# Performance work log

Hardware: AMD Instinct MI355X
Metric: run time of the kernel (lower is better)

## Reference

```python
import jax, jax.numpy as jnp
import numpy as np

DIM = 384
NUM_HEADS = 6
HEAD_DIM = DIM // NUM_HEADS
SCALE = HEAD_DIM ** -0.5


def setup_inputs() -> dict:
    key = jax.random.key(0)
    k_x, k_wqkv, k_bqkv, k_wp, k_bp = jax.random.split(key, 5)
    B, N, D = 16, 1024, DIM
    s = 0.02
    return {
        "x": jax.random.normal(k_x, (B, N, D), dtype=jnp.float32),
        "w_qkv": jax.random.normal(k_wqkv, (D, 3 * D), dtype=jnp.float32) * s,
        "b_qkv": jax.random.normal(k_bqkv, (3 * D,), dtype=jnp.float32) * s,
        "w_proj": jax.random.normal(k_wp, (D, D), dtype=jnp.float32) * s,
        "b_proj": jax.random.normal(k_bp, (D,), dtype=jnp.float32) * s,
    }


def reference(x, w_qkv, b_qkv, w_proj, b_proj):
    b, n, d = x.shape
    qkv = x @ w_qkv + b_qkv                               # (B, N, 3D)
    qkv = qkv.reshape(b, n, 3, NUM_HEADS, HEAD_DIM)
    qkv = jnp.transpose(qkv, (2, 0, 3, 1, 4))             # (3, B, H, N, hd)
    q, k, v = qkv[0], qkv[1], qkv[2]
    attn = jnp.einsum("bhqd,bhkd->bhqk", q, k) * SCALE    # (B, H, N, N)
    attn = jax.nn.softmax(attn, axis=-1)
    out = jnp.einsum("bhqk,bhkd->bhqd", attn, v)          # (B, H, N, hd)
    out = jnp.transpose(out, (0, 2, 1, 3)).reshape(b, n, d)
    return out @ w_proj + b_proj
```

## Files before the change

### kernel.cpp

```cpp
#include <hip/hip_runtime.h>

typedef __attribute__((ext_vector_type(8))) short short8;
typedef __attribute__((ext_vector_type(4))) float float4_t;
typedef __attribute__((ext_vector_type(4))) unsigned int uint4_t;

#define MFMA16(A, B, C) __builtin_amdgcn_mfma_f32_16x16x32_bf16(A, B, C, 0, 0, 0)

__device__ __forceinline__ unsigned short f2bf(float f) {
  unsigned int u = __builtin_bit_cast(unsigned int, f);
  u += 0x7FFFu + ((u >> 16) & 1u);
  return (unsigned short)(u >> 16);
}

__device__ __forceinline__ void gload16(const unsigned short* g, unsigned short* l) {
  __builtin_amdgcn_global_load_lds(
      (const __attribute__((address_space(1))) unsigned int*)(g),
      (__attribute__((address_space(3))) unsigned int*)(l), 16, 0, 0);
}

__global__ __launch_bounds__(256) void prep(
    const float* __restrict__ x, const float* __restrict__ w_qkv,
    const float* __restrict__ w_proj, unsigned short* __restrict__ xb,
    unsigned short* __restrict__ wqkvT, unsigned short* __restrict__ wprojT) {
  __shared__ unsigned short tile[32][33];
  const int bid = blockIdx.x, tid = threadIdx.x;
  if (bid < 6144) {
    const int i = bid * 256 + tid;
    float4 v = reinterpret_cast<const float4*>(x)[i];
    ushort4 r;
    r.x = f2bf(v.x); r.y = f2bf(v.y); r.z = f2bf(v.z); r.w = f2bf(v.w);
    reinterpret_cast<ushort4*>(xb)[i] = r;
    return;
  }
  const float* w; unsigned short* wT; int E, t;
  if (bid < 6576) { t = bid - 6144; w = w_qkv; wT = wqkvT; E = 1152; }
  else            { t = bid - 6576; w = w_proj; wT = wprojT; E = 384; }
  const int tiles_e = E >> 5;
  const int td = t / tiles_e, te = t - td * tiles_e;
  const int r = tid >> 3, c4 = (tid & 7) * 4;
  float4 v = *reinterpret_cast<const float4*>(&w[(size_t)(td * 32 + r) * E + te * 32 + c4]);
  tile[r][c4 + 0] = f2bf(v.x);
  tile[r][c4 + 1] = f2bf(v.y);
  tile[r][c4 + 2] = f2bf(v.z);
  tile[r][c4 + 3] = f2bf(v.w);
  __syncthreads();
  ushort4 o;
  o.x = tile[c4 + 0][r]; o.y = tile[c4 + 1][r];
  o.z = tile[c4 + 2][r]; o.w = tile[c4 + 3][r];
  *reinterpret_cast<ushort4*>(&wT[(size_t)(te * 32 + r) * 384 + td * 32 + c4]) = o;
}

__global__ __launch_bounds__(256, 2) void gemm_qkv(
    const unsigned short* __restrict__ xb,
    const unsigned short* __restrict__ wT,
    const float* __restrict__ bias,
    unsigned short* __restrict__ qb,
    unsigned short* __restrict__ kb,
    unsigned short* __restrict__ vt) {
  __shared__ alignas(16) char smem[65536];
  const int tid = threadIdx.x;
  const int wg = (blockIdx.x & 7) * 144 + (blockIdx.x >> 3);
  const int bm = wg / 9, bn = wg - bm * 9;
  const int m0 = bm * 128, n0 = bn * 128;
  const int lane = tid & 63, wid = tid >> 6;
  const int lr = lane & 15, lg = lane >> 4;
  const int wm = wid >> 1, wn = wid & 1;
  float4_t acc[4][4] = {};

  const unsigned short* asrc[4];
  const unsigned short* bsrc[4];
  int dstoff[4];
#pragma unroll
  for (int i = 0; i < 4; ++i) {
    const int idx = tid + i * 256;
    const int r = idx >> 3, c8 = idx & 7;
    const int cc = (c8 ^ (r & 7)) * 8;
    asrc[i] = xb + (size_t)(m0 + r) * 384 + cc;
    bsrc[i] = wT + (size_t)(n0 + r) * 384 + cc;
    dstoff[i] = idx * 16;
  }
  const int rxor = (lr & 7) << 4;

#pragma unroll
  for (int i = 0; i < 4; ++i) {
    gload16(asrc[i], (unsigned short*)(smem + dstoff[i]));
    gload16(bsrc[i], (unsigned short*)(smem + 32768 + dstoff[i]));
  }
  __syncthreads();

#pragma unroll
  for (int kt = 0; kt < 6; ++kt) {
    const int cur = kt & 1;
    if (kt < 5) {
      const int nb = (cur ^ 1) * 16384;
#pragma unroll
      for (int i = 0; i < 4; ++i) {
        gload16(asrc[i] + (kt + 1) * 64, (unsigned short*)(smem + nb + dstoff[i]));
        gload16(bsrc[i] + (kt + 1) * 64, (unsigned short*)(smem + 32768 + nb + dstoff[i]));
      }
    }
    const char* Ab = smem + cur * 16384;
    const char* Bb = smem + 32768 + cur * 16384;
#pragma unroll
    for (int kk = 0; kk < 2; ++kk) {
      short8 a[4], b[4];
#pragma unroll
      for (int f = 0; f < 4; ++f) {
        a[f] = *reinterpret_cast<const short8*>(
            Ab + (wm * 64 + f * 16 + lr) * 128 + ((kk * 64 + lg * 16) ^ rxor));
        b[f] = *reinterpret_cast<const short8*>(
            Bb + (wn * 64 + f * 16 + lr) * 128 + ((kk * 64 + lg * 16) ^ rxor));
      }
#pragma unroll
      for (int mf = 0; mf < 4; ++mf)
#pragma unroll
        for (int nf = 0; nf < 4; ++nf)
          acc[mf][nf] = MFMA16(a[mf], b[nf], acc[mf][nf]);
    }
    __syncthreads();
  }

#pragma unroll
  for (int nf = 0; nf < 4; ++nf) {
    const int e = n0 + wn * 64 + nf * 16 + lr;
    const float bv = bias[e];
    const int which = e / 384;
    const int d = e - which * 384;
    const int h = d >> 6, hi = d & 63;
#pragma unroll
    for (int mf = 0; mf < 4; ++mf) {
      const int mm0 = m0 + wm * 64 + mf * 16 + lg * 4;
      const int b0 = mm0 >> 10, n_b = mm0 & 1023;
      const size_t bh = (size_t)(b0 * 6 + h);
      if (which == 2) {
        const int np = (n_b & ~31) | ((n_b & 12) << 1) | ((n_b & 16) >> 2);
        ushort4 sv;
        sv.x = f2bf(acc[mf][nf][0] + bv);
        sv.y = f2bf(acc[mf][nf][1] + bv);
        sv.z = f2bf(acc[mf][nf][2] + bv);
        sv.w = f2bf(acc[mf][nf][3] + bv);
        *reinterpret_cast<ushort4*>(&vt[bh * 65536 + (size_t)hi * 1024 + np]) = sv;
      } else {
        unsigned short* dst = (which == 0) ? qb : kb;
#pragma unroll
        for (int j = 0; j < 4; ++j) {
          float val = acc[mf][nf][j] + bv;
          if (which == 0) val *= 0.125f;
          dst[bh * 65536 + (size_t)(n_b + j) * 64 + hi] = f2bf(val);
        }
      }
    }
  }
}

__global__ __launch_bounds__(256, 6) void attn(
    const unsigned short* __restrict__ qb,
    const unsigned short* __restrict__ kb,
    const unsigned short* __restrict__ vt,
    unsigned short* __restrict__ ab) {
  __shared__ alignas(16) char smem[16384];
  const int tid = threadIdx.x;
  const int wg = (blockIdx.x & 7) * 192 + (blockIdx.x >> 3);
  const int bh = wg >> 4, qt = wg & 15;
  const int lane = tid & 63, wid = tid >> 6;
  const int lr = lane & 15, lg = lane >> 4;
  const size_t base = (size_t)bh * 65536;
  const unsigned short* qp = qb + base;
  const unsigned short* kp = kb + base;
  const unsigned short* vp = vt + base;
  const int q0 = qt * 64 + wid * 16;

  short8 aq0 = *reinterpret_cast<const short8*>(&qp[(size_t)(q0 + lr) * 64 + lg * 8]);
  short8 aq1 = *reinterpret_cast<const short8*>(&qp[(size_t)(q0 + lr) * 64 + 32 + lg * 8]);

  const int rK = tid >> 3;
  const int cK = (((tid & 7) * 16) ^ ((rK & 7) << 4)) >> 1;
  const int rV = tid >> 2;
  const int cV = (((tid & 3) * 16) ^ ((rV & 3) << 4)) >> 1;
  const unsigned short* ksrc = kp + rK * 64 + cK;
  const unsigned short* vsrc = vp + rV * 1024 + cV;
  unsigned short* kdst0 = (unsigned short*)(smem + wid * 1024);
  unsigned short* vdst0 = (unsigned short*)(smem + 8192 + wid * 1024);

  const int kxor = (lr & 7) << 4;
  const int vxor = (lr & 3) << 4;

  float lsum = 0.f;
  float4_t o[4] = {};

  gload16(ksrc, kdst0);
  gload16(vsrc, vdst0);
  __syncthreads();

  for (int kt = 0; kt < 32; ++kt) {
    const int cur = kt & 1;
    if (kt < 31) {
      const int nb = (cur ^ 1) * 4096;
      gload16(ksrc + (kt + 1) * 2048, (unsigned short*)((char*)kdst0 + nb));
      gload16(vsrc + (kt + 1) * 32, (unsigned short*)((char*)vdst0 + nb));
    }
    const char* kbase = smem + cur * 4096;
    const char* vbase = smem + 8192 + cur * 4096;

    short8 bk[2][2], bv[4];
#pragma unroll
    for (int kf = 0; kf < 2; ++kf)
#pragma unroll
      for (int h = 0; h < 2; ++h)
        bk[kf][h] = *reinterpret_cast<const short8*>(
            kbase + (kf * 16 + lr) * 128 + ((h * 64 + lg * 16) ^ kxor));
#pragma unroll
    for (int f = 0; f < 4; ++f)
      bv[f] = *reinterpret_cast<const short8*>(
          vbase + (f * 16 + lr) * 64 + ((lg * 16) ^ vxor));

    float4_t s[2] = {};
#pragma unroll
    for (int kf = 0; kf < 2; ++kf) {
      s[kf] = MFMA16(bk[kf][0], aq0, s[kf]);
      s[kf] = MFMA16(bk[kf][1], aq1, s[kf]);
    }
    unsigned int dw[4];
#pragma unroll
    for (int kf = 0; kf < 2; ++kf) {
      const float p0 = __expf(s[kf][0]);
      const float p1 = __expf(s[kf][1]);
      const float p2 = __expf(s[kf][2]);
      const float p3 = __expf(s[kf][3]);
      lsum += (p0 + p1) + (p2 + p3);
      dw[kf * 2]     = (unsigned int)f2bf(p0) | ((unsigned int)f2bf(p1) << 16);
      dw[kf * 2 + 1] = (unsigned int)f2bf(p2) | ((unsigned int)f2bf(p3) << 16);
    }
    uint4_t pw;
    pw[0] = dw[0]; pw[1] = dw[1]; pw[2] = dw[2]; pw[3] = dw[3];
    const short8 pa = __builtin_bit_cast(short8, pw);
#pragma unroll
    for (int f = 0; f < 4; ++f)
      o[f] = MFMA16(pa, bv[f], o[f]);

    __syncthreads();
  }

  float t = lsum;
  t += __shfl_xor(t, 16);
  t += __shfl_xor(t, 32);
  const float inv = 1.f / t;

  const int b = bh / 6, h = bh - b * 6;
  float invj[4];
#pragma unroll
  for (int j = 0; j < 4; ++j)
    invj[j] = __shfl(inv, lg * 4 + j);
#pragma unroll
  for (int f = 0; f < 4; ++f)
#pragma unroll
    for (int j = 0; j < 4; ++j) {
      const int q = q0 + lg * 4 + j;
      ab[(size_t)(b * 1024 + q) * 384 + h * 64 + f * 16 + lr] =
          f2bf(o[f][j] * invj[j]);
    }
}

__global__ __launch_bounds__(256, 3) void gemm_proj(
    const unsigned short* __restrict__ ab,
    const unsigned short* __restrict__ wT,
    const float* __restrict__ bias,
    float* __restrict__ out) {
  __shared__ alignas(16) char smem[49152];
  const int tid = threadIdx.x;
  const int wg = (blockIdx.x & 7) * 96 + (blockIdx.x >> 3);
  const int bm = wg / 3, bn = wg - bm * 3;
  const int m0 = bm * 64, n0 = bn * 128;
  const int lane = tid & 63, wid = tid >> 6;
  const int lr = lane & 15, lg = lane >> 4;
  const int wm = wid >> 1, wn = wid & 1;
  float4_t acc[2][4] = {};

  const unsigned short* asrc[2];
  const unsigned short* bsrc[4];
  int adst[2], bdst[4];
#pragma unroll
  for (int i = 0; i < 2; ++i) {
    const int idx = tid + i * 256;
    const int r = idx >> 3, c8 = idx & 7;
    asrc[i] = ab + (size_t)(m0 + r) * 384 + (c8 ^ (r & 7)) * 8;
    adst[i] = idx * 16;
  }
#pragma unroll
  for (int i = 0; i < 4; ++i) {
    const int idx = tid + i * 256;
    const int r = idx >> 3, c8 = idx & 7;
    bsrc[i] = wT + (size_t)(n0 + r) * 384 + (c8 ^ (r & 7)) * 8;
    bdst[i] = idx * 16;
  }
  const int rxor = (lr & 7) << 4;

#pragma unroll
  for (int i = 0; i < 2; ++i) gload16(asrc[i], (unsigned short*)(smem + adst[i]));
#pragma unroll
  for (int i = 0; i < 4; ++i) gload16(bsrc[i], (unsigned short*)(smem + 16384 + bdst[i]));
  __syncthreads();

#pragma unroll
  for (int kt = 0; kt < 6; ++kt) {
    const int cur = kt & 1;
    if (kt < 5) {
#pragma unroll
      for (int i = 0; i < 2; ++i)
        gload16(asrc[i] + (kt + 1) * 64, (unsigned short*)(smem + (cur ^ 1) * 8192 + adst[i]));
#pragma unroll
      for (int i = 0; i < 4; ++i)
        gload16(bsrc[i] + (kt + 1) * 64, (unsigned short*)(smem + 16384 + (cur ^ 1) * 16384 + bdst[i]));
    }
    const char* Ab = smem + cur * 8192;
    const char* Bb = smem + 16384 + cur * 16384;
#pragma unroll
    for (int kk = 0; kk < 2; ++kk) {
      short8 a[2], b[4];
#pragma unroll
      for (int f = 0; f < 2; ++f)
        a[f] = *reinterpret_cast<const short8*>(
            Ab + (wm * 32 + f * 16 + lr) * 128 + ((kk * 64 + lg * 16) ^ rxor));
#pragma unroll
      for (int f = 0; f < 4; ++f)
        b[f] = *reinterpret_cast<const short8*>(
            Bb + (wn * 64 + f * 16 + lr) * 128 + ((kk * 64 + lg * 16) ^ rxor));
#pragma unroll
      for (int mf = 0; mf < 2; ++mf)
#pragma unroll
        for (int nf = 0; nf < 4; ++nf)
          acc[mf][nf] = MFMA16(a[mf], b[nf], acc[mf][nf]);
    }
    __syncthreads();
  }

#pragma unroll
  for (int nf = 0; nf < 4; ++nf) {
    const int e = n0 + wn * 64 + nf * 16 + lr;
    const float bv = bias[e];
#pragma unroll
    for (int mf = 0; mf < 2; ++mf) {
#pragma unroll
      for (int j = 0; j < 4; ++j) {
        const int mm = m0 + wm * 32 + mf * 16 + lg * 4 + j;
        out[(size_t)mm * 384 + e] = acc[mf][nf][j] + bv;
      }
    }
  }
}

extern "C" void kernel_launch(void* const* d_in, const int* in_sizes, int n_in,
                              void* d_out, int out_size, void* d_ws, size_t ws_size,
                              hipStream_t stream) {
  const float* x      = (const float*)d_in[0];
  const float* w_qkv  = (const float*)d_in[1];
  const float* b_qkv  = (const float*)d_in[2];
  const float* w_proj = (const float*)d_in[3];
  const float* b_proj = (const float*)d_in[4];
  float* out = (float*)d_out;

  char* ws = (char*)d_ws;
  unsigned short* xb     = (unsigned short*)(ws);
  unsigned short* wqkvT  = (unsigned short*)(ws + 12582912);
  unsigned short* wprojT = (unsigned short*)(ws + 13467648);
  unsigned short* qb     = (unsigned short*)(ws + 13762560);
  unsigned short* kb     = (unsigned short*)(ws + 26345472);
  unsigned short* vt     = (unsigned short*)(ws + 38928384);
  unsigned short* ab     = xb;

  prep<<<6720, 256, 0, stream>>>(x, w_qkv, w_proj, xb, wqkvT, wprojT);
  gemm_qkv<<<1152, 256, 0, stream>>>(xb, wqkvT, b_qkv, qb, kb, vt);
  attn<<<1536, 256, 0, stream>>>(qb, kb, vt, ab);
  gemm_proj<<<768, 256, 0, stream>>>(ab, wprojT, b_proj, out);
}
```

Measured before the change: 96.11 us.

## Vectorize QKV/proj epilogues, enlarge attention tiles, use exp2 and packed bf16 conversion

In the QKV and projection GEMMs, the MFMA operands are swapped for Q/K and the output tiles so each lane holds four consecutive columns, letting the epilogues issue 8-byte bf16 and 16-byte float stores with a vector bias load. The attention kernel moves to 512-thread blocks covering 128 queries and 64-key tiles, which halves the number of K/V loads and barriers per query. Q is prescaled by log2(e)/8 so the softmax can use the hardware exp2 directly. Probabilities are packed with v_cvt_pk_bf16_f32, and the row sum is taken from the rounded bf16 values. The larger blocks double LDS use and change occupancy, and the unnormalized exp with no max subtraction is kept.

```diff
diff --git a/kernel.cpp b/kernel.cpp
--- a/kernel.cpp
+++ b/kernel.cpp
@@ -5,6 +5,8 @@
 typedef __attribute__((ext_vector_type(4))) unsigned int uint4_t;
 
 #define MFMA16(A, B, C) __builtin_amdgcn_mfma_f32_16x16x32_bf16(A, B, C, 0, 0, 0)
+
+#define QSCALE 0.1803368801111168f
 
 __device__ __forceinline__ unsigned short f2bf(float f) {
   unsigned int u = __builtin_bit_cast(unsigned int, f);
@@ -111,133 +113,166 @@
         b[f] = *reinterpret_cast<const short8*>(
             Bb + (wn * 64 + f * 16 + lr) * 128 + ((kk * 64 + lg * 16) ^ rxor));
       }
-#pragma unroll
-      for (int mf = 0; mf < 4; ++mf)
-#pragma unroll
-        for (int nf = 0; nf < 4; ++nf)
-          acc[mf][nf] = MFMA16(a[mf], b[nf], acc[mf][nf]);
+      if (bn < 6) {
+#pragma unroll
+        for (int mf = 0; mf < 4; ++mf)
+#pragma unroll
+          for (int nf = 0; nf < 4; ++nf)
+            acc[mf][nf] = MFMA16(b[nf], a[mf], acc[mf][nf]);
+      } else {
+#pragma unroll
+        for (int mf = 0; mf < 4; ++mf)
+#pragma unroll
+          for (int nf = 0; nf < 4; ++nf)
+            acc[mf][nf] = MFMA16(a[mf], b[nf], acc[mf][nf]);
+      }
     }
     __syncthreads();
   }
 
-#pragma unroll
-  for (int nf = 0; nf < 4; ++nf) {
-    const int e = n0 + wn * 64 + nf * 16 + lr;
-    const float bv = bias[e];
-    const int which = e / 384;
-    const int d = e - which * 384;
-    const int h = d >> 6, hi = d & 63;
-#pragma unroll
-    for (int mf = 0; mf < 4; ++mf) {
-      const int mm0 = m0 + wm * 64 + mf * 16 + lg * 4;
-      const int b0 = mm0 >> 10, n_b = mm0 & 1023;
-      const size_t bh = (size_t)(b0 * 6 + h);
-      if (which == 2) {
+  if (bn < 6) {
+    const int whichk = (bn >= 3);
+    unsigned short* dst = whichk ? kb : qb;
+    const float sc = whichk ? 1.f : QSCALE;
+#pragma unroll
+    for (int nf = 0; nf < 4; ++nf) {
+      const int e0 = n0 + wn * 64 + nf * 16 + lg * 4;
+      const int d0 = e0 - whichk * 384;
+      const int h = d0 >> 6, hi0 = d0 & 63;
+      const float4 bv4 = *reinterpret_cast<const float4*>(&bias[e0]);
+#pragma unroll
+      for (int mf = 0; mf < 4; ++mf) {
+        const int mm = m0 + wm * 64 + mf * 16 + lr;
+        const int b0 = mm >> 10, n_b = mm & 1023;
+        const size_t bhh = (size_t)(b0 * 6 + h);
+        ushort4 sv;
+        sv.x = f2bf((acc[mf][nf][0] + bv4.x) * sc);
+        sv.y = f2bf((acc[mf][nf][1] + bv4.y) * sc);
+        sv.z = f2bf((acc[mf][nf][2] + bv4.z) * sc);
+        sv.w = f2bf((acc[mf][nf][3] + bv4.w) * sc);
+        *reinterpret_cast<ushort4*>(&dst[bhh * 65536 + (size_t)n_b * 64 + hi0]) = sv;
+      }
+    }
+  } else {
+#pragma unroll
+    for (int nf = 0; nf < 4; ++nf) {
+      const int e = n0 + wn * 64 + nf * 16 + lr;
+      const float bv = bias[e];
+      const int d = e - 768;
+      const int h = d >> 6, hi = d & 63;
+#pragma unroll
+      for (int mf = 0; mf < 4; ++mf) {
+        const int mm0 = m0 + wm * 64 + mf * 16 + lg * 4;
+        const int b0 = mm0 >> 10, n_b = mm0 & 1023;
+        const size_t bhh = (size_t)(b0 * 6 + h);
         const int np = (n_b & ~31) | ((n_b & 12) << 1) | ((n_b & 16) >> 2);
         ushort4 sv;
         sv.x = f2bf(acc[mf][nf][0] + bv);
         sv.y = f2bf(acc[mf][nf][1] + bv);
         sv.z = f2bf(acc[mf][nf][2] + bv);
         sv.w = f2bf(acc[mf][nf][3] + bv);
-        *reinterpret_cast<ushort4*>(&vt[bh * 65536 + (size_t)hi * 1024 + np]) = sv;
-      } else {
-        unsigned short* dst = (which == 0) ? qb : kb;
-#pragma unroll
-        for (int j = 0; j < 4; ++j) {
-          float val = acc[mf][nf][j] + bv;
-          if (which == 0) val *= 0.125f;
-          dst[bh * 65536 + (size_t)(n_b + j) * 64 + hi] = f2bf(val);
-        }
-      }
-    }
-  }
-}
-
-__global__ __launch_bounds__(256, 6) void attn(
+        *reinterpret_cast<ushort4*>(&vt[bhh * 65536 + (size_t)hi * 1024 + np]) = sv;
+      }
+    }
+  }
+}
+
+__global__ __launch_bounds__(512, 6) void attn(
     const unsigned short* __restrict__ qb,
     const unsigned short* __restrict__ kb,
     const unsigned short* __restrict__ vt,
     unsigned short* __restrict__ ab) {
-  __shared__ alignas(16) char smem[16384];
+  __shared__ alignas(16) char smem[32768];
   const int tid = threadIdx.x;
-  const int wg = (blockIdx.x & 7) * 192 + (blockIdx.x >> 3);
-  const int bh = wg >> 4, qt = wg & 15;
+  const int wg = (blockIdx.x & 7) * 96 + (blockIdx.x >> 3);
+  const int bh = wg >> 3, qt = wg & 7;
   const int lane = tid & 63, wid = tid >> 6;
   const int lr = lane & 15, lg = lane >> 4;
   const size_t base = (size_t)bh * 65536;
   const unsigned short* qp = qb + base;
   const unsigned short* kp = kb + base;
   const unsigned short* vp = vt + base;
-  const int q0 = qt * 64 + wid * 16;
+  const int q0 = qt * 128 + wid * 16;
 
   short8 aq0 = *reinterpret_cast<const short8*>(&qp[(size_t)(q0 + lr) * 64 + lg * 8]);
   short8 aq1 = *reinterpret_cast<const short8*>(&qp[(size_t)(q0 + lr) * 64 + 32 + lg * 8]);
 
-  const int rK = tid >> 3;
-  const int cK = (((tid & 7) * 16) ^ ((rK & 7) << 4)) >> 1;
-  const int rV = tid >> 2;
-  const int cV = (((tid & 3) * 16) ^ ((rV & 3) << 4)) >> 1;
-  const unsigned short* ksrc = kp + rK * 64 + cK;
-  const unsigned short* vsrc = vp + rV * 1024 + cV;
-  unsigned short* kdst0 = (unsigned short*)(smem + wid * 1024);
-  unsigned short* vdst0 = (unsigned short*)(smem + 8192 + wid * 1024);
-
-  const int kxor = (lr & 7) << 4;
-  const int vxor = (lr & 3) << 4;
+  const int rr = tid >> 3;
+  const int cc = (((tid & 7) * 16) ^ ((rr & 7) << 4)) >> 1;
+  const unsigned short* ksrc = kp + rr * 64 + cc;
+  const unsigned short* vsrc = vp + rr * 1024 + cc;
+  unsigned short* kdst = (unsigned short*)(smem + tid * 16);
+  unsigned short* vdst = (unsigned short*)(smem + 16384 + tid * 16);
+
+  const int xr = (lr & 7) << 4;
 
   float lsum = 0.f;
   float4_t o[4] = {};
 
-  gload16(ksrc, kdst0);
-  gload16(vsrc, vdst0);
+  gload16(ksrc, kdst);
+  gload16(vsrc, vdst);
   __syncthreads();
 
-  for (int kt = 0; kt < 32; ++kt) {
+  for (int kt = 0; kt < 16; ++kt) {
     const int cur = kt & 1;
-    if (kt < 31) {
-      const int nb = (cur ^ 1) * 4096;
-      gload16(ksrc + (kt + 1) * 2048, (unsigned short*)((char*)kdst0 + nb));
-      gload16(vsrc + (kt + 1) * 32, (unsigned short*)((char*)vdst0 + nb));
-    }
-    const char* kbase = smem + cur * 4096;
-    const char* vbase = smem + 8192 + cur * 4096;
-
-    short8 bk[2][2], bv[4];
-#pragma unroll
-    for (int kf = 0; kf < 2; ++kf)
-#pragma unroll
-      for (int h = 0; h < 2; ++h)
-        bk[kf][h] = *reinterpret_cast<const short8*>(
-            kbase + (kf * 16 + lr) * 128 + ((h * 64 + lg * 16) ^ kxor));
-#pragma unroll
-    for (int f = 0; f < 4; ++f)
-      bv[f] = *reinterpret_cast<const short8*>(
-          vbase + (f * 16 + lr) * 64 + ((lg * 16) ^ vxor));
-
-    float4_t s[2] = {};
-#pragma unroll
-    for (int kf = 0; kf < 2; ++kf) {
-      s[kf] = MFMA16(bk[kf][0], aq0, s[kf]);
-      s[kf] = MFMA16(bk[kf][1], aq1, s[kf]);
-    }
-    unsigned int dw[4];
-#pragma unroll
-    for (int kf = 0; kf < 2; ++kf) {
-      const float p0 = __expf(s[kf][0]);
-      const float p1 = __expf(s[kf][1]);
-      const float p2 = __expf(s[kf][2]);
-      const float p3 = __expf(s[kf][3]);
-      lsum += (p0 + p1) + (p2 + p3);
-      dw[kf * 2]     = (unsigned int)f2bf(p0) | ((unsigned int)f2bf(p1) << 16);
-      dw[kf * 2 + 1] = (unsigned int)f2bf(p2) | ((unsigned int)f2bf(p3) << 16);
-    }
-    uint4_t pw;
-    pw[0] = dw[0]; pw[1] = dw[1]; pw[2] = dw[2]; pw[3] = dw[3];
-    const short8 pa = __builtin_bit_cast(short8, pw);
-#pragma unroll
-    for (int f = 0; f < 4; ++f)
-      o[f] = MFMA16(pa, bv[f], o[f]);
-
+    if (kt < 15) {
+      const int nb = (cur ^ 1) * 8192;
+      gload16(ksrc + (kt + 1) * 4096, (unsigned short*)(smem + nb + tid * 16));
+      gload16(vsrc + (kt + 1) * 64, (unsigned short*)(smem + 16384 + nb + tid * 16));
+    }
+    const char* kbase = smem + cur * 8192;
+    const char* vbase = smem + 16384 + cur * 8192;
+
+#pragma unroll
+    for (int half = 0; half < 2; ++half) {
+      short8 bk00 = *reinterpret_cast<const short8*>(
+          kbase + (half * 32 + lr) * 128 + ((lg * 16) ^ xr));
+      short8 bk01 = *reinterpret_cast<const short8*>(
+          kbase + (half * 32 + lr) * 128 + ((64 + lg * 16) ^ xr));
+      short8 bk10 = *reinterpret_cast<const short8*>(
+          kbase + (half * 32 + 16 + lr) * 128 + ((lg * 16) ^ xr));
+      short8 bk11 = *reinterpret_cast<const short8*>(
+          kbase + (half * 32 + 16 + lr) * 128 + ((64 + lg * 16) ^ xr));
+      float4_t s0 = {}, s1 = {};
+      s0 = MFMA16(bk00, aq0, s0);
+      s0 = MFMA16(bk01, aq1, s0);
+      s1 = MFMA16(bk10, aq0, s1);
+      s1 = MFMA16(bk11, aq1, s1);
+
+      unsigned int dw0, dw1, dw2, dw3;
+      {
+        const float p0 = __builtin_amdgcn_exp2f(s0[0]);
+        const float p1 = __builtin_amdgcn_exp2f(s0[1]);
+        const float p2 = __builtin_amdgcn_exp2f(s0[2]);
+        const float p3 = __builtin_amdgcn_exp2f(s0[3]);
+        asm("v_cvt_pk_bf16_f32 %0, %1, %2" : "=v"(dw0) : "v"(p0), "v"(p1));
+        asm("v_cvt_pk_bf16_f32 %0, %1, %2" : "=v"(dw1) : "v"(p2), "v"(p3));
+        const float p4 = __builtin_amdgcn_exp2f(s1[0]);
+        const float p5 = __builtin_amdgcn_exp2f(s1[1]);
+        const float p6 = __builtin_amdgcn_exp2f(s1[2]);
+        const float p7 = __builtin_amdgcn_exp2f(s1[3]);
+        asm("v_cvt_pk_bf16_f32 %0, %1, %2" : "=v"(dw2) : "v"(p4), "v"(p5));
+        asm("v_cvt_pk_bf16_f32 %0, %1, %2" : "=v"(dw3) : "v"(p6), "v"(p7));
+      }
+      lsum += __builtin_bit_cast(float, dw0 << 16) +
+              __builtin_bit_cast(float, dw0 & 0xFFFF0000u) +
+              __builtin_bit_cast(float, dw1 << 16) +
+              __builtin_bit_cast(float, dw1 & 0xFFFF0000u) +
+              __builtin_bit_cast(float, dw2 << 16) +
+              __builtin_bit_cast(float, dw2 & 0xFFFF0000u) +
+              __builtin_bit_cast(float, dw3 << 16) +
+              __builtin_bit_cast(float, dw3 & 0xFFFF0000u);
+
+      uint4_t pw;
+      pw[0] = dw0; pw[1] = dw1; pw[2] = dw2; pw[3] = dw3;
+      const short8 pa = __builtin_bit_cast(short8, pw);
+#pragma unroll
+      for (int f = 0; f < 4; ++f) {
+        short8 bv = *reinterpret_cast<const short8*>(
+            vbase + (f * 16 + lr) * 128 + ((half * 64 + lg * 16) ^ xr));
+        o[f] = MFMA16(pa, bv, o[f]);
+      }
+    }
     __syncthreads();
   }
 
@@ -329,22 +364,24 @@
       for (int mf = 0; mf < 2; ++mf)
 #pragma unroll
         for (int nf = 0; nf < 4; ++nf)
-          acc[mf][nf] = MFMA16(a[mf], b[nf], acc[mf][nf]);
+          acc[mf][nf] = MFMA16(b[nf], a[mf], acc[mf][nf]);
     }
     __syncthreads();
   }
 
 #pragma unroll
   for (int nf = 0; nf < 4; ++nf) {
-    const int e = n0 + wn * 64 + nf * 16 + lr;
-    const float bv = bias[e];
+    const int e0 = n0 + wn * 64 + nf * 16 + lg * 4;
+    const float4 bv4 = *reinterpret_cast<const float4*>(&bias[e0]);
 #pragma unroll
     for (int mf = 0; mf < 2; ++mf) {
-#pragma unroll
-      for (int j = 0; j < 4; ++j) {
-        const int mm = m0 + wm * 32 + mf * 16 + lg * 4 + j;
-        out[(size_t)mm * 384 + e] = acc[mf][nf][j] + bv;
-      }
+      const int mm = m0 + wm * 32 + mf * 16 + lr;
+      float4 ov;
+      ov.x = acc[mf][nf][0] + bv4.x;
+      ov.y = acc[mf][nf][1] + bv4.y;
+      ov.z = acc[mf][nf][2] + bv4.z;
+      ov.w = acc[mf][nf][3] + bv4.w;
+      *reinterpret_cast<float4*>(&out[(size_t)mm * 384 + e0]) = ov;
     }
   }
 }
@@ -370,6 +407,6 @@
 
   prep<<<6720, 256, 0, stream>>>(x, w_qkv, w_proj, xb, wqkvT, wprojT);
   gemm_qkv<<<1152, 256, 0, stream>>>(xb, wqkvT, b_qkv, qb, kb, vt);
-  attn<<<1536, 256, 0, stream>>>(qb, kb, vt, ab);
+  attn<<<768, 512, 0, stream>>>(qb, kb, vt, ab);
   gemm_proj<<<768, 256, 0, stream>>>(ab, wprojT, b_proj, out);
 }
```

Result: faster. 87.17 us (-9.3%).
